# Kernel tuning notes

Hardware: AMD Instinct MI355X
Metric: run time of the kernel (lower is better)

## Reference

```python
import jax, jax.numpy as jnp
import numpy as np

N = 100000      # nodes
E = 3200000     # edges (before self-loops)
IN = 1          # input feature dim
H1, C = 4, 8    # layer1: 4 heads x 8 channels; layer2: 1 head x 8 channels
NEG_SLOPE = 0.2


def setup_inputs() -> dict:
    key = jax.random.key(0)
    ks = jax.random.split(key, 10)
    x = jax.random.normal(ks[0], (N, IN), jnp.float32)
    edge_index = jax.random.randint(ks[1], (2, E), 0, N, dtype=jnp.int32)
    # layer 1 params (GATConv(1, 8, heads=4))
    W1 = jax.random.normal(ks[2], (IN, H1 * C), jnp.float32) * 0.5
    a_src1 = jax.random.normal(ks[3], (H1, C), jnp.float32) * 0.5
    a_dst1 = jax.random.normal(ks[4], (H1, C), jnp.float32) * 0.5
    b1 = jnp.zeros((H1 * C,), jnp.float32)
    # layer 2 params (GATConv(32, 8, heads=1))
    W2 = jax.random.normal(ks[5], (H1 * C, C), jnp.float32) * 0.2
    a_src2 = jax.random.normal(ks[6], (1, C), jnp.float32) * 0.5
    a_dst2 = jax.random.normal(ks[7], (1, C), jnp.float32) * 0.5
    b2 = jnp.zeros((C,), jnp.float32)
    return {"x": x, "edge_index": edge_index, "W1": W1, "a_src1": a_src1,
            "a_dst1": a_dst1, "b1": b1, "W2": W2, "a_src2": a_src2,
            "a_dst2": a_dst2, "b2": b2}


def _gat_layer(x, src, dst, W, a_s, a_d, b, heads, ch):
    # Linear transform per head: [N, heads, ch]
    h = (x @ W).reshape(-1, heads, ch)
    # per-node attention logits
    al_s = jnp.einsum('nhc,hc->nh', h, a_s)  # [N, H]
    al_d = jnp.einsum('nhc,hc->nh', h, a_d)  # [N, H]
    # per-edge logits (message src -> dst)
    e = jax.nn.leaky_relu(al_s[src] + al_d[dst], NEG_SLOPE)  # [E', H]
    # segment softmax over incoming edges of each dst node
    m = jax.ops.segment_max(e, dst, num_segments=N)          # [N, H]
    e = jnp.exp(e - m[dst])
    s = jax.ops.segment_sum(e, dst, num_segments=N)          # [N, H]
    alpha = e / s[dst]                                       # [E', H]
    # weighted scatter-add aggregation
    out = jax.ops.segment_sum(h[src] * alpha[:, :, None], dst, num_segments=N)
    return out.reshape(N, heads * ch) + b


def reference(x, edge_index, W1, a_src1, a_dst1, b1, W2, a_src2, a_dst2, b2):
    loops = jnp.arange(N, dtype=edge_index.dtype)
    src = jnp.concatenate([edge_index[0], loops])  # add self-loops (PyG default)
    dst = jnp.concatenate([edge_index[1], loops])
    h = _gat_layer(x, src, dst, W1, a_src1, a_dst1, b1, H1, C)
    h = jax.nn.relu(h)
    out = _gat_layer(h, src, dst, W2, a_src2, a_dst2, b2, 1, C)
    return out
```

## Files before the change

### kernel.cpp

```cpp
#include <hip/hip_runtime.h>
#include <hip/hip_bf16.h>

#define NEG_SLOPE 0.2f
#define CAP   6144
#define CAPG  8192
#define CAPA  81920


__global__ void init_cc(int* __restrict__ curA, int* __restrict__ curB,
                        const float* __restrict__ W1,
                        const float* __restrict__ as1,
                        const float* __restrict__ ad1,
                        float* __restrict__ consts) {
    int t = threadIdx.x;
    if (t < 8) {
        int h = t & 3;
        const float* a = (t < 4) ? as1 : ad1;
        float s = 0.f;
        #pragma unroll
        for (int c = 0; c < 8; ++c)
            s += W1[h * 8 + c] * a[h * 8 + c];
        consts[t] = s;
    }
    if (t < 64) curA[t] = t * CAPA;
    curB[t] = t << 13;
}

__global__ void scatterA(const int* __restrict__ ei, int* __restrict__ curA,
                         unsigned int* __restrict__ bufA, int E) {
    __shared__ int cnt[64];
    __shared__ int basel[64];
    int t = threadIdx.x;
    int chunk = (E + gridDim.x - 1) / gridDim.x;
    int lo = blockIdx.x * chunk;
    int hi = min(E, lo + chunk);
    const int* dei = ei + E;
    if (t < 64) cnt[t] = 0;
    __syncthreads();
    bool vec = ((E & 3) == 0);
    int lo4 = (lo + 3) & ~3;
    int end4 = hi & ~3;
    if (vec && end4 > lo4) {
        for (int e = lo + t; e < lo4; e += 1024)
            atomicAdd(&cnt[dei[e] >> 11], 1);
        const int4* dei4 = (const int4*)dei;
        for (int v = (lo4 >> 2) + t; v < (end4 >> 2); v += 1024) {
            int4 d = dei4[v];
            atomicAdd(&cnt[d.x >> 11], 1);
            atomicAdd(&cnt[d.y >> 11], 1);
            atomicAdd(&cnt[d.z >> 11], 1);
            atomicAdd(&cnt[d.w >> 11], 1);
        }
        for (int e = end4 + t; e < hi; e += 1024)
            atomicAdd(&cnt[dei[e] >> 11], 1);
    } else {
        for (int e = lo + t; e < hi; e += 1024)
            atomicAdd(&cnt[dei[e] >> 11], 1);
    }
    __syncthreads();
    if (t < 64) {
        int c = cnt[t];
        basel[t] = c ? (atomicAdd(&curA[t], c) - t * CAPA) : 0;
        cnt[t] = 0;
    }
    __syncthreads();
    if (vec && end4 > lo4) {
        for (int e = lo + t; e < lo4; e += 1024) {
            int s = ei[e], d = dei[e];
            int sp = d >> 11;
            int off = basel[sp] + atomicAdd(&cnt[sp], 1);
            if (off < CAPA) bufA[sp * CAPA + off] = (unsigned)s | ((unsigned)(d & 2047) << 17);
        }
        const int4* sei4 = (const int4*)ei;
        const int4* dei4 = (const int4*)dei;
        for (int v = (lo4 >> 2) + t; v < (end4 >> 2); v += 1024) {
            int4 sv = sei4[v];
            int4 dv = dei4[v];
            int s0 = dv.x >> 11, s1 = dv.y >> 11, s2 = dv.z >> 11, s3 = dv.w >> 11;
            int o0 = basel[s0] + atomicAdd(&cnt[s0], 1);
            if (o0 < CAPA) bufA[s0 * CAPA + o0] = (unsigned)sv.x | ((unsigned)(dv.x & 2047) << 17);
            int o1 = basel[s1] + atomicAdd(&cnt[s1], 1);
            if (o1 < CAPA) bufA[s1 * CAPA + o1] = (unsigned)sv.y | ((unsigned)(dv.y & 2047) << 17);
            int o2 = basel[s2] + atomicAdd(&cnt[s2], 1);
            if (o2 < CAPA) bufA[s2 * CAPA + o2] = (unsigned)sv.z | ((unsigned)(dv.z & 2047) << 17);
            int o3 = basel[s3] + atomicAdd(&cnt[s3], 1);
            if (o3 < CAPA) bufA[s3 * CAPA + o3] = (unsigned)sv.w | ((unsigned)(dv.w & 2047) << 17);
        }
        for (int e = end4 + t; e < hi; e += 1024) {
            int s = ei[e], d = dei[e];
            int sp = d >> 11;
            int off = basel[sp] + atomicAdd(&cnt[sp], 1);
            if (off < CAPA) bufA[sp * CAPA + off] = (unsigned)s | ((unsigned)(d & 2047) << 17);
        }
    } else {
        for (int e = lo + t; e < hi; e += 1024) {
            int s = ei[e], d = dei[e];
            int sp = d >> 11;
            int off = basel[sp] + atomicAdd(&cnt[sp], 1);
            if (off < CAPA) bufA[sp * CAPA + off] = (unsigned)s | ((unsigned)(d & 2047) << 17);
        }
    }
}

__global__ void scatterB(const int* __restrict__ curA, int* __restrict__ curB,
                         const unsigned int* __restrict__ bufA,
                         unsigned int* __restrict__ pairs) {
    __shared__ int cnt[16];
    __shared__ int basel[16];
    int t = threadIdx.x;
    int sp = blockIdx.x >> 3;
    int part = blockIdx.x & 7;
    int base = sp * CAPA;
    int fill = min(curA[sp] - base, CAPA);
    if (fill <= 0) return;
    int lo = (fill * part) >> 3;
    int hi = (fill * (part + 1)) >> 3;
    for (int c0 = lo; c0 < hi; c0 += 8192) {
        int cend = min(hi, c0 + 8192);
        if (t < 16) cnt[t] = 0;
        __syncthreads();
        for (int i = c0 + t; i < cend; i += 1024)
            atomicAdd(&cnt[(bufA[base + i] >> 24) & 15], 1);
        __syncthreads();
        if (t < 16) {
            int c = cnt[t];
            int bkg = (sp << 4) + t;
            basel[t] = c ? (atomicAdd(&curB[bkg], c) - (bkg << 13)) : 0;
            cnt[t] = 0;
        }
        __syncthreads();
        for (int i = c0 + t; i < cend; i += 1024) {
            unsigned p = bufA[base + i];
            int b16 = (p >> 24) & 15;
            int off = basel[b16] + atomicAdd(&cnt[b16], 1);
            if (off < CAPG) {
                int bkg = (sp << 4) + b16;
                pairs[(bkg << 13) + off] = p & 0x00FFFFFFu;
            }
        }
        __syncthreads();
    }
}

__global__ __launch_bounds__(1024, 8)
void l1_comb(const float* __restrict__ x,
             const int* __restrict__ curB,
             const unsigned int* __restrict__ pairs,
             const float* __restrict__ consts,
             const float* __restrict__ W1, const float* __restrict__ b1,
             const float* __restrict__ W2,
             const float* __restrict__ as2, const float* __restrict__ ad2,
             float* __restrict__ h2, float* __restrict__ als2,
             float* __restrict__ ald2, int N) {
    __shared__ unsigned sbuf[CAP];
    __shared__ int hcnt[128], offs[128], hcur[128];
    __shared__ float xl[128];
    int t = threadIdx.x;
    int bk = blockIdx.x;
    int node0 = bk << 7;
    int nw = min(128, N - node0);
    if (t < 128) xl[t] = (t < nw) ? x[node0 + t] : 0.f;
    float S[4], D[4];
    #pragma unroll
    for (int h = 0; h < 4; ++h) { S[h] = consts[h]; D[h] = consts[4 + h]; }
    int base = bk << 13;
    int cnt_total = min(curB[bk] - base, CAPG);
    int g = t >> 3, j = t & 7;
    float sacc[4] = {0.f, 0.f, 0.f, 0.f};
    float tacc[4] = {0.f, 0.f, 0.f, 0.f};
    __syncthreads();
    float xd = xl[g];
    for (int c0 = 0; c0 < cnt_total; c0 += CAP) {
        int clen = min(CAP, cnt_total - c0);
        unsigned pr[6];
        #pragma unroll
        for (int k = 0; k < 6; ++k) {
            int idx = t + (k << 10);
            pr[k] = (idx < clen) ? pairs[base + c0 + idx] : 0xFFFFFFFFu;
        }
        if (t < 128) hcnt[t] = 0;
        __syncthreads();
        #pragma unroll
        for (int k = 0; k < 6; ++k)
            if (pr[k] != 0xFFFFFFFFu) atomicAdd(&hcnt[pr[k] >> 17], 1);
        __syncthreads();
        if (t < 64) {
            int h0 = hcnt[2 * t], h1 = hcnt[2 * t + 1];
            int s = h0 + h1, sc_ = s;
            #pragma unroll
            for (int o = 1; o < 64; o <<= 1) {
                int u = __shfl_up(sc_, o);
                if (t >= o) sc_ += u;
            }
            int excl = sc_ - s;
            offs[2 * t] = excl;          hcur[2 * t] = excl;
            offs[2 * t + 1] = excl + h0; hcur[2 * t + 1] = excl + h0;
        }
        __syncthreads();
        #pragma unroll
        for (int k = 0; k < 6; ++k)
            if (pr[k] != 0xFFFFFFFFu) {
                int loc = atomicAdd(&hcur[pr[k] >> 17], 1);
                sbuf[loc] = pr[k];
            }
        __syncthreads();
        int st = offs[g], en = st + hcnt[g];
        int i = st + j;
        float xs0 = 0.f, xs1 = 0.f;
        if (i < en) xs0 = x[sbuf[i] & 131071u];
        if (i + 8 < en) xs1 = x[sbuf[i + 8] & 131071u];
        for (; i < en; i += 8) {
            float xs = xs0;
            xs0 = xs1;
            int i2 = i + 16;
            xs1 = (i2 < en) ? x[sbuf[i2] & 131071u] : 0.f;
            #pragma unroll
            for (int h = 0; h < 4; ++h) {
                float v = xs * S[h] + xd * D[h];
                v = (v > 0.f) ? v : NEG_SLOPE * v;
                float w = __expf(v);
                sacc[h] += w;
                tacc[h] = fmaf(w, xs, tacc[h]);
            }
        }
        __syncthreads();
    }
    #pragma unroll
    for (int h = 0; h < 4; ++h) {
        sacc[h] += __shfl_xor(sacc[h], 1); sacc[h] += __shfl_xor(sacc[h], 2);
        sacc[h] += __shfl_xor(sacc[h], 4);
        tacc[h] += __shfl_xor(tacc[h], 1); tacc[h] += __shfl_xor(tacc[h], 2);
        tacc[h] += __shfl_xor(tacc[h], 4);
    }
    if (j == 0 && g < nw) {
        int n = node0 + g;
        float xn = xd;
        float o[8];
        #pragma unroll
        for (int c = 0; c < 8; ++c) o[c] = 0.f;
        #pragma unroll
        for (int h = 0; h < 4; ++h) {
            float v = xn * (S[h] + D[h]);
            v = (v > 0.f) ? v : NEG_SLOPE * v;
            float ww = __expf(v);
            float s1 = ww + sacc[h];
            float t1 = ww * xn + tacc[h];
            float tt = t1 / s1;
            #pragma unroll
            for (int c = 0; c < 8; ++c) {
                float rr = fmaxf(tt * W1[h * 8 + c] + b1[h * 8 + c], 0.f);
                #pragma unroll
                for (int c2 = 0; c2 < 8; ++c2) o[c2] += rr * W2[(h * 8 + c) * 8 + c2];
            }
        }
        float as = 0.f, ad = 0.f;
        #pragma unroll
        for (int c = 0; c < 8; ++c) { as += o[c] * as2[c]; ad += o[c] * ad2[c]; }
        float4* hv = (float4*)&h2[(size_t)n * 8];
        hv[0] = make_float4(o[0], o[1], o[2], o[3]);
        hv[1] = make_float4(o[4], o[5], o[6], o[7]);
        als2[n] = as;
        ald2[n] = ad;
    }
}

__global__ __launch_bounds__(1024, 8)
void l2_comb(const int* __restrict__ curB,
             const unsigned int* __restrict__ pairs,
             const float* __restrict__ als2, const float* __restrict__ ald2,
             const float* __restrict__ h2, const float* __restrict__ b2,
             float* __restrict__ out, int N) {
    __shared__ unsigned sbuf[CAP];
    __shared__ int hcnt[128], offs[128], hcur[128];
    __shared__ float adl[128];
    int t = threadIdx.x;
    int bk = blockIdx.x;
    int node0 = bk << 7;
    int nw = min(128, N - node0);
    if (t < 128) adl[t] = (t < nw) ? ald2[node0 + t] : 0.f;
    int base = bk << 13;
    int cnt_total = min(curB[bk] - base, CAPG);
    int g = t >> 3, j = t & 7;
    float acc[9];
    #pragma unroll
    for (int c = 0; c < 9; ++c) acc[c] = 0.f;
    __syncthreads();
    float adv = adl[g];
    for (int c0 = 0; c0 < cnt_total; c0 += CAP) {
        int clen = min(CAP, cnt_total - c0);
        unsigned pr[6];
        #pragma unroll
        for (int k = 0; k < 6; ++k) {
            int idx = t + (k << 10);
            pr[k] = (idx < clen) ? pairs[base + c0 + idx] : 0xFFFFFFFFu;
        }
        if (t < 128) hcnt[t] = 0;
        __syncthreads();
        #pragma unroll
        for (int k = 0; k < 6; ++k)
            if (pr[k] != 0xFFFFFFFFu) atomicAdd(&hcnt[pr[k] >> 17], 1);
        __syncthreads();
        if (t < 64) {
            int h0 = hcnt[2 * t], h1 = hcnt[2 * t + 1];
            int s = h0 + h1, sc_ = s;
            #pragma unroll
            for (int o = 1; o < 64; o <<= 1) {
                int u = __shfl_up(sc_, o);
                if (t >= o) sc_ += u;
            }
            int excl = sc_ - s;
            offs[2 * t] = excl;          hcur[2 * t] = excl;
            offs[2 * t + 1] = excl + h0; hcur[2 * t + 1] = excl + h0;
        }
        __syncthreads();
        #pragma unroll
        for (int k = 0; k < 6; ++k)
            if (pr[k] != 0xFFFFFFFFu) {
                int loc = atomicAdd(&hcur[pr[k] >> 17], 1);
                sbuf[loc] = pr[k];
            }
        __syncthreads();
        int st = offs[g], en = st + hcnt[g];
        int i = st + j;
        float a0 = 0.f, a1 = 0.f;
        float4 hA0 = make_float4(0,0,0,0), hB0 = hA0, hA1 = hA0, hB1 = hA0;
        if (i < en) {
            int s0 = (int)(sbuf[i] & 131071u);
            a0 = als2[s0];
            const float4* q = (const float4*)&h2[(size_t)s0 * 8];
            hA0 = q[0]; hB0 = q[1];
        }
        if (i + 8 < en) {
            int s1 = (int)(sbuf[i + 8] & 131071u);
            a1 = als2[s1];
            const float4* q = (const float4*)&h2[(size_t)s1 * 8];
            hA1 = q[0]; hB1 = q[1];
        }
        for (; i < en; i += 8) {
            float a = a0; float4 hA = hA0, hB = hB0;
            a0 = a1; hA0 = hA1; hB0 = hB1;
            int i2 = i + 16;
            if (i2 < en) {
                int s2 = (int)(sbuf[i2] & 131071u);
                a1 = als2[s2];
                const float4* q = (const float4*)&h2[(size_t)s2 * 8];
                hA1 = q[0]; hB1 = q[1];
            } else {
                a1 = 0.f;
            }
            float v = a + adv;
            v = (v > 0.f) ? v : NEG_SLOPE * v;
            float w = __expf(v);
            acc[0] += w;
            acc[1] = fmaf(w, hA.x, acc[1]); acc[2] = fmaf(w, hA.y, acc[2]);
            acc[3] = fmaf(w, hA.z, acc[3]); acc[4] = fmaf(w, hA.w, acc[4]);
            acc[5] = fmaf(w, hB.x, acc[5]); acc[6] = fmaf(w, hB.y, acc[6]);
            acc[7] = fmaf(w, hB.z, acc[7]); acc[8] = fmaf(w, hB.w, acc[8]);
        }
        __syncthreads();
    }
    #pragma unroll
    for (int c = 0; c < 9; ++c) {
        acc[c] += __shfl_xor(acc[c], 1);
        acc[c] += __shfl_xor(acc[c], 2);
        acc[c] += __shfl_xor(acc[c], 4);
    }
    if (j == 0 && g < nw) {
        int n = node0 + g;
        float v = als2[n] + adv;
        v = (v > 0.f) ? v : NEG_SLOPE * v;
        float ww = __expf(v);
        const float4* hv = (const float4*)&h2[(size_t)n * 8];
        float4 ha0 = hv[0], hb0 = hv[1];
        float s2v = acc[0] + ww;
        float inv = 1.f / s2v;
        float4* ov = (float4*)&out[(size_t)n * 8];
        ov[0] = make_float4((acc[1] + ww * ha0.x) * inv + b2[0],
                            (acc[2] + ww * ha0.y) * inv + b2[1],
                            (acc[3] + ww * ha0.z) * inv + b2[2],
                            (acc[4] + ww * ha0.w) * inv + b2[3]);
        ov[1] = make_float4((acc[5] + ww * hb0.x) * inv + b2[4],
                            (acc[6] + ww * hb0.y) * inv + b2[5],
                            (acc[7] + ww * hb0.z) * inv + b2[6],
                            (acc[8] + ww * hb0.w) * inv + b2[7]);
    }
}


__global__ void prep_consts(const float* __restrict__ W1,
                            const float* __restrict__ as1,
                            const float* __restrict__ ad1,
                            float* __restrict__ consts) {
    int t = threadIdx.x;
    if (t >= 8) return;
    int h = t & 3;
    const float* a = (t < 4) ? as1 : ad1;
    float s = 0.f;
    #pragma unroll
    for (int c = 0; c < 8; ++c)
        s += W1[h * 8 + c] * a[h * 8 + c];
    consts[t] = s;
}

__global__ void edge_pass1(const int* __restrict__ ei, const float* __restrict__ x,
                           const float* __restrict__ consts,
                           float* __restrict__ s1, float* __restrict__ t1, int E, int N) {
    int e = blockIdx.x * blockDim.x + threadIdx.x;
    if (e >= E + N) return;
    int src, dst;
    if (e < E) { src = ei[e]; dst = ei[E + e]; }
    else       { src = dst = e - E; }
    float xs = x[src], xd = x[dst];
    #pragma unroll
    for (int h = 0; h < 4; ++h) {
        float v = xs * consts[h] + xd * consts[4 + h];
        v = (v > 0.f) ? v : NEG_SLOPE * v;
        float w = __expf(v);
        atomicAdd(&s1[dst * 4 + h], w);
        atomicAdd(&t1[dst * 4 + h], w * xs);
    }
}

__global__ void node_mid(const float* __restrict__ s1, const float* __restrict__ t1,
                         const float* __restrict__ W1, const float* __restrict__ b1,
                         const float* __restrict__ W2,
                         const float* __restrict__ as2, const float* __restrict__ ad2,
                         float* __restrict__ h2, float* __restrict__ als2,
                         float* __restrict__ ald2, int N) {
    int n = blockIdx.x * blockDim.x + threadIdx.x;
    if (n >= N) return;
    float o[8];
    #pragma unroll
    for (int c = 0; c < 8; ++c) o[c] = 0.f;
    #pragma unroll
    for (int h = 0; h < 4; ++h) {
        float t = t1[n * 4 + h] / s1[n * 4 + h];
        #pragma unroll
        for (int c = 0; c < 8; ++c) {
            float r = fmaxf(t * W1[h * 8 + c] + b1[h * 8 + c], 0.f);
            #pragma unroll
            for (int c2 = 0; c2 < 8; ++c2) o[c2] += r * W2[(h * 8 + c) * 8 + c2];
        }
    }
    float as = 0.f, ad = 0.f;
    #pragma unroll
    for (int c = 0; c < 8; ++c) { h2[n * 8 + c] = o[c]; as += o[c] * as2[c]; ad += o[c] * ad2[c]; }
    als2[n] = as; ald2[n] = ad;
}

__global__ void edge_pass2(const int* __restrict__ ei, const float* __restrict__ als2,
                           const float* __restrict__ ald2, const float* __restrict__ h2,
                           float* __restrict__ s2, float* __restrict__ acc2, int E, int N) {
    int e = blockIdx.x * blockDim.x + threadIdx.x;
    if (e >= E + N) return;
    int src, dst;
    if (e < E) { src = ei[e]; dst = ei[E + e]; }
    else       { src = dst = e - E; }
    float v = als2[src] + ald2[dst];
    v = (v > 0.f) ? v : NEG_SLOPE * v;
    float w = __expf(v);
    atomicAdd(&s2[dst], w);
    const float4* hs = (const float4*)&h2[src * 8];
    float4 a = hs[0], bq = hs[1];
    float* acc = &acc2[dst * 8];
    atomicAdd(&acc[0], w * a.x);  atomicAdd(&acc[1], w * a.y);
    atomicAdd(&acc[2], w * a.z);  atomicAdd(&acc[3], w * a.w);
    atomicAdd(&acc[4], w * bq.x); atomicAdd(&acc[5], w * bq.y);
    atomicAdd(&acc[6], w * bq.z); atomicAdd(&acc[7], w * bq.w);
}

__global__ void node_out(const float* __restrict__ s2, const float* __restrict__ acc2,
                         const float* __restrict__ b2, float* __restrict__ out, int N) {
    int i = blockIdx.x * blockDim.x + threadIdx.x;
    if (i >= N * 8) return;
    out[i] = acc2[i] / s2[i >> 3] + b2[i & 7];
}


extern "C" void kernel_launch(void* const* d_in, const int* in_sizes, int n_in,
                              void* d_out, int out_size, void* d_ws, size_t ws_size,
                              hipStream_t stream) {
    const float* x   = (const float*)d_in[0];
    const int*   ei  = (const int*)d_in[1];
    const float* W1  = (const float*)d_in[2];
    const float* as1 = (const float*)d_in[3];
    const float* ad1 = (const float*)d_in[4];
    const float* b1  = (const float*)d_in[5];
    const float* W2  = (const float*)d_in[6];
    const float* as2 = (const float*)d_in[7];
    const float* ad2 = (const float*)d_in[8];
    const float* b2  = (const float*)d_in[9];
    float* out = (float*)d_out;

    const int N = in_sizes[0];
    const int E = in_sizes[1] / 2;
    const int NBK = (N + 127) >> 7;

    float* ws = (float*)d_ws;
    size_t need = (size_t)(16 + 64 + 1024 + 10 * (size_t)N
                           + (size_t)1024 * CAPG + (size_t)64 * CAPA) * sizeof(float);

    if (N <= 131072 && ws_size >= need) {
        float*    consts = ws;
        int*      curA   = (int*)(ws + 16);
        int*      curB   = curA + 64;
        float*    als2   = ws + 16 + 64 + 1024;
        float*    ald2   = als2 + N;
        float*    h2     = ald2 + N;
        unsigned* pairs  = (unsigned*)(h2 + 8 * (size_t)N);
        unsigned* bufA   = pairs + (size_t)1024 * CAPG;

        init_cc<<<1, 1024, 0, stream>>>(curA, curB, W1, as1, ad1, consts);
        scatterA<<<256, 1024, 0, stream>>>(ei, curA, bufA, E);
        scatterB<<<512, 1024, 0, stream>>>(curA, curB, bufA, pairs);
        l1_comb<<<NBK, 1024, 0, stream>>>(x, curB, pairs, consts,
                                          W1, b1, W2, as2, ad2, h2, als2, ald2, N);
        l2_comb<<<NBK, 1024, 0, stream>>>(curB, pairs, als2, ald2, h2, b2, out, N);
    } else {
        float* consts = ws;
        float* s1   = ws + 16;
        float* t1   = s1 + 4 * (size_t)N;
        float* h2   = t1 + 4 * (size_t)N;
        float* als2 = h2 + 8 * (size_t)N;
        float* ald2 = als2 + (size_t)N;
        float* s2   = ald2 + (size_t)N;
        float* acc2 = s2 + (size_t)N;

        hipMemsetAsync(ws, 0, (16 + 8 * (size_t)N) * sizeof(float), stream);
        hipMemsetAsync(s2, 0, 9 * (size_t)N * sizeof(float), stream);
        prep_consts<<<1, 64, 0, stream>>>(W1, as1, ad1, consts);
        int total = E + N;
        edge_pass1<<<(total + 255) / 256, 256, 0, stream>>>(ei, x, consts, s1, t1, E, N);
        node_mid<<<(N + 255) / 256, 256, 0, stream>>>(s1, t1, W1, b1, W2, as2, ad2, h2, als2, ald2, N);
        edge_pass2<<<(total + 255) / 256, 256, 0, stream>>>(ei, als2, ald2, h2, s2, acc2, E, N);
        node_out<<<(N * 8 + 255) / 256, 256, 0, stream>>>(s2, acc2, b2, out, N);
    }
}
```

Baseline: 201.5 us.

## Fuse GAT pipeline into one cooperative kernel with grid syncs and reuse sorted edges

Merges the five separate launches (init, two scatter passes, layer-1 and layer-2 combines) into a single cooperative kernel separated by grid-wide syncs. Layer 1 now saves its per-block sorted edge lists and per-node offset/count metadata to global memory, so layer 2 reads them directly instead of re-histogramming and re-sorting in shared memory. The per-block chunk is enlarged to hold a full bucket in one pass. In exchange it adds grid-sync overhead, a persistent grid of 256 or 512 blocks looping over buckets, an occupancy query on the host, and a larger shared buffer that may reduce occupancy.

```diff
diff --git a/kernel.cpp b/kernel.cpp
--- a/kernel.cpp
+++ b/kernel.cpp
@@ -1,187 +1,177 @@
 #include <hip/hip_runtime.h>
+#include <hip/hip_cooperative_groups.h>
 #include <hip/hip_bf16.h>
 
+namespace cg = cooperative_groups;
+
 #define NEG_SLOPE 0.2f
-#define CAP   6144
-#define CAPG  8192
-#define CAPA  81920
-
-
-__global__ void init_cc(int* __restrict__ curA, int* __restrict__ curB,
-                        const float* __restrict__ W1,
-                        const float* __restrict__ as1,
-                        const float* __restrict__ ad1,
-                        float* __restrict__ consts) {
+#define CAPG 8192
+#define CAPA 81920
+
+
+__global__ __launch_bounds__(1024, 8)
+void fused_gat(const float* __restrict__ x, const int* __restrict__ ei,
+               const float* __restrict__ W1, const float* __restrict__ as1,
+               const float* __restrict__ ad1, const float* __restrict__ b1,
+               const float* __restrict__ W2, const float* __restrict__ as2,
+               const float* __restrict__ ad2, const float* __restrict__ b2,
+               float* __restrict__ out,
+               int* __restrict__ curA, int* __restrict__ curB,
+               unsigned* __restrict__ bufA, unsigned* __restrict__ pairs,
+               unsigned* __restrict__ gsorted, int* __restrict__ bmeta,
+               float* __restrict__ als2, float* __restrict__ ald2,
+               float* __restrict__ h2,
+               int E, int N, int nbk)
+{
+    cg::grid_group grid = cg::this_grid();
+    __shared__ unsigned sbuf[CAPG];
+    __shared__ int hcnt[128], offs[128], hcur[128];
+    __shared__ int cntA[64], baseA[64];
+    __shared__ int cntB[16], baseB[16];
+    __shared__ float xl[128];
+
     int t = threadIdx.x;
-    if (t < 8) {
-        int h = t & 3;
-        const float* a = (t < 4) ? as1 : ad1;
-        float s = 0.f;
-        #pragma unroll
-        for (int c = 0; c < 8; ++c)
-            s += W1[h * 8 + c] * a[h * 8 + c];
-        consts[t] = s;
-    }
-    if (t < 64) curA[t] = t * CAPA;
-    curB[t] = t << 13;
-}
-
-__global__ void scatterA(const int* __restrict__ ei, int* __restrict__ curA,
-                         unsigned int* __restrict__ bufA, int E) {
-    __shared__ int cnt[64];
-    __shared__ int basel[64];
-    int t = threadIdx.x;
-    int chunk = (E + gridDim.x - 1) / gridDim.x;
-    int lo = blockIdx.x * chunk;
-    int hi = min(E, lo + chunk);
-    const int* dei = ei + E;
-    if (t < 64) cnt[t] = 0;
-    __syncthreads();
-    bool vec = ((E & 3) == 0);
-    int lo4 = (lo + 3) & ~3;
-    int end4 = hi & ~3;
-    if (vec && end4 > lo4) {
-        for (int e = lo + t; e < lo4; e += 1024)
-            atomicAdd(&cnt[dei[e] >> 11], 1);
-        const int4* dei4 = (const int4*)dei;
-        for (int v = (lo4 >> 2) + t; v < (end4 >> 2); v += 1024) {
-            int4 d = dei4[v];
-            atomicAdd(&cnt[d.x >> 11], 1);
-            atomicAdd(&cnt[d.y >> 11], 1);
-            atomicAdd(&cnt[d.z >> 11], 1);
-            atomicAdd(&cnt[d.w >> 11], 1);
-        }
-        for (int e = end4 + t; e < hi; e += 1024)
-            atomicAdd(&cnt[dei[e] >> 11], 1);
-    } else {
-        for (int e = lo + t; e < hi; e += 1024)
-            atomicAdd(&cnt[dei[e] >> 11], 1);
-    }
-    __syncthreads();
-    if (t < 64) {
-        int c = cnt[t];
-        basel[t] = c ? (atomicAdd(&curA[t], c) - t * CAPA) : 0;
-        cnt[t] = 0;
-    }
-    __syncthreads();
-    if (vec && end4 > lo4) {
-        for (int e = lo + t; e < lo4; e += 1024) {
-            int s = ei[e], d = dei[e];
-            int sp = d >> 11;
-            int off = basel[sp] + atomicAdd(&cnt[sp], 1);
-            if (off < CAPA) bufA[sp * CAPA + off] = (unsigned)s | ((unsigned)(d & 2047) << 17);
-        }
-        const int4* sei4 = (const int4*)ei;
-        const int4* dei4 = (const int4*)dei;
-        for (int v = (lo4 >> 2) + t; v < (end4 >> 2); v += 1024) {
-            int4 sv = sei4[v];
-            int4 dv = dei4[v];
-            int s0 = dv.x >> 11, s1 = dv.y >> 11, s2 = dv.z >> 11, s3 = dv.w >> 11;
-            int o0 = basel[s0] + atomicAdd(&cnt[s0], 1);
-            if (o0 < CAPA) bufA[s0 * CAPA + o0] = (unsigned)sv.x | ((unsigned)(dv.x & 2047) << 17);
-            int o1 = basel[s1] + atomicAdd(&cnt[s1], 1);
-            if (o1 < CAPA) bufA[s1 * CAPA + o1] = (unsigned)sv.y | ((unsigned)(dv.y & 2047) << 17);
-            int o2 = basel[s2] + atomicAdd(&cnt[s2], 1);
-            if (o2 < CAPA) bufA[s2 * CAPA + o2] = (unsigned)sv.z | ((unsigned)(dv.z & 2047) << 17);
-            int o3 = basel[s3] + atomicAdd(&cnt[s3], 1);
-            if (o3 < CAPA) bufA[s3 * CAPA + o3] = (unsigned)sv.w | ((unsigned)(dv.w & 2047) << 17);
-        }
-        for (int e = end4 + t; e < hi; e += 1024) {
-            int s = ei[e], d = dei[e];
-            int sp = d >> 11;
-            int off = basel[sp] + atomicAdd(&cnt[sp], 1);
-            if (off < CAPA) bufA[sp * CAPA + off] = (unsigned)s | ((unsigned)(d & 2047) << 17);
-        }
-    } else {
-        for (int e = lo + t; e < hi; e += 1024) {
-            int s = ei[e], d = dei[e];
-            int sp = d >> 11;
-            int off = basel[sp] + atomicAdd(&cnt[sp], 1);
-            if (off < CAPA) bufA[sp * CAPA + off] = (unsigned)s | ((unsigned)(d & 2047) << 17);
-        }
-    }
-}
-
-__global__ void scatterB(const int* __restrict__ curA, int* __restrict__ curB,
-                         const unsigned int* __restrict__ bufA,
-                         unsigned int* __restrict__ pairs) {
-    __shared__ int cnt[16];
-    __shared__ int basel[16];
-    int t = threadIdx.x;
-    int sp = blockIdx.x >> 3;
-    int part = blockIdx.x & 7;
-    int base = sp * CAPA;
-    int fill = min(curA[sp] - base, CAPA);
-    if (fill <= 0) return;
-    int lo = (fill * part) >> 3;
-    int hi = (fill * (part + 1)) >> 3;
-    for (int c0 = lo; c0 < hi; c0 += 8192) {
-        int cend = min(hi, c0 + 8192);
-        if (t < 16) cnt[t] = 0;
-        __syncthreads();
-        for (int i = c0 + t; i < cend; i += 1024)
-            atomicAdd(&cnt[(bufA[base + i] >> 24) & 15], 1);
-        __syncthreads();
-        if (t < 16) {
-            int c = cnt[t];
-            int bkg = (sp << 4) + t;
-            basel[t] = c ? (atomicAdd(&curB[bkg], c) - (bkg << 13)) : 0;
-            cnt[t] = 0;
-        }
-        __syncthreads();
-        for (int i = c0 + t; i < cend; i += 1024) {
-            unsigned p = bufA[base + i];
-            int b16 = (p >> 24) & 15;
-            int off = basel[b16] + atomicAdd(&cnt[b16], 1);
-            if (off < CAPG) {
-                int bkg = (sp << 4) + b16;
-                pairs[(bkg << 13) + off] = p & 0x00FFFFFFu;
-            }
-        }
-        __syncthreads();
-    }
-}
-
-__global__ __launch_bounds__(1024, 8)
-void l1_comb(const float* __restrict__ x,
-             const int* __restrict__ curB,
-             const unsigned int* __restrict__ pairs,
-             const float* __restrict__ consts,
-             const float* __restrict__ W1, const float* __restrict__ b1,
-             const float* __restrict__ W2,
-             const float* __restrict__ as2, const float* __restrict__ ad2,
-             float* __restrict__ h2, float* __restrict__ als2,
-             float* __restrict__ ald2, int N) {
-    __shared__ unsigned sbuf[CAP];
-    __shared__ int hcnt[128], offs[128], hcur[128];
-    __shared__ float xl[128];
-    int t = threadIdx.x;
-    int bk = blockIdx.x;
-    int node0 = bk << 7;
-    int nw = min(128, N - node0);
-    if (t < 128) xl[t] = (t < nw) ? x[node0 + t] : 0.f;
+    int B = blockIdx.x;
+    int G = gridDim.x;
+
     float S[4], D[4];
     #pragma unroll
-    for (int h = 0; h < 4; ++h) { S[h] = consts[h]; D[h] = consts[4 + h]; }
-    int base = bk << 13;
-    int cnt_total = min(curB[bk] - base, CAPG);
-    int g = t >> 3, j = t & 7;
-    float sacc[4] = {0.f, 0.f, 0.f, 0.f};
-    float tacc[4] = {0.f, 0.f, 0.f, 0.f};
-    __syncthreads();
-    float xd = xl[g];
-    for (int c0 = 0; c0 < cnt_total; c0 += CAP) {
-        int clen = min(CAP, cnt_total - c0);
-        unsigned pr[6];
-        #pragma unroll
-        for (int k = 0; k < 6; ++k) {
+    for (int h = 0; h < 4; ++h) {
+        float s = 0.f, d = 0.f;
+        #pragma unroll
+        for (int c = 0; c < 8; ++c) {
+            float w = W1[h * 8 + c];
+            s += w * as1[h * 8 + c];
+            d += w * ad1[h * 8 + c];
+        }
+        S[h] = s; D[h] = d;
+    }
+
+    if (B == 0) {
+        if (t < 64) curA[t] = t * CAPA;
+        curB[t] = t << 13;
+    }
+    __threadfence();
+    grid.sync();
+
+    {
+        int chunk = (E + G - 1) / G;
+        int lo = B * chunk;
+        int hi = min(E, lo + chunk);
+        const int* dei = ei + E;
+        if (t < 64) cntA[t] = 0;
+        __syncthreads();
+        bool vec = ((E & 3) == 0);
+        int lo4 = (lo + 3) & ~3;
+        int end4 = hi & ~3;
+        if (vec && end4 > lo4) {
+            for (int e = lo + t; e < lo4; e += 1024) atomicAdd(&cntA[dei[e] >> 11], 1);
+            const int4* dei4 = (const int4*)dei;
+            for (int v = (lo4 >> 2) + t; v < (end4 >> 2); v += 1024) {
+                int4 d = dei4[v];
+                atomicAdd(&cntA[d.x >> 11], 1); atomicAdd(&cntA[d.y >> 11], 1);
+                atomicAdd(&cntA[d.z >> 11], 1); atomicAdd(&cntA[d.w >> 11], 1);
+            }
+            for (int e = end4 + t; e < hi; e += 1024) atomicAdd(&cntA[dei[e] >> 11], 1);
+        } else {
+            for (int e = lo + t; e < hi; e += 1024) atomicAdd(&cntA[dei[e] >> 11], 1);
+        }
+        __syncthreads();
+        if (t < 64) {
+            int c = cntA[t];
+            baseA[t] = c ? (atomicAdd(&curA[t], c) - t * CAPA) : 0;
+            cntA[t] = 0;
+        }
+        __syncthreads();
+        if (vec && end4 > lo4) {
+            for (int e = lo + t; e < lo4; e += 1024) {
+                int s = ei[e], d = dei[e]; int sp = d >> 11;
+                int off = baseA[sp] + atomicAdd(&cntA[sp], 1);
+                if (off < CAPA) bufA[sp * CAPA + off] = (unsigned)s | ((unsigned)(d & 2047) << 17);
+            }
+            const int4* sei4 = (const int4*)ei;
+            const int4* dei4 = (const int4*)dei;
+            for (int v = (lo4 >> 2) + t; v < (end4 >> 2); v += 1024) {
+                int4 sv = sei4[v]; int4 dv = dei4[v];
+                int s0 = dv.x >> 11, s1 = dv.y >> 11, s2 = dv.z >> 11, s3 = dv.w >> 11;
+                int o0 = baseA[s0] + atomicAdd(&cntA[s0], 1);
+                if (o0 < CAPA) bufA[s0 * CAPA + o0] = (unsigned)sv.x | ((unsigned)(dv.x & 2047) << 17);
+                int o1 = baseA[s1] + atomicAdd(&cntA[s1], 1);
+                if (o1 < CAPA) bufA[s1 * CAPA + o1] = (unsigned)sv.y | ((unsigned)(dv.y & 2047) << 17);
+                int o2 = baseA[s2] + atomicAdd(&cntA[s2], 1);
+                if (o2 < CAPA) bufA[s2 * CAPA + o2] = (unsigned)sv.z | ((unsigned)(dv.z & 2047) << 17);
+                int o3 = baseA[s3] + atomicAdd(&cntA[s3], 1);
+                if (o3 < CAPA) bufA[s3 * CAPA + o3] = (unsigned)sv.w | ((unsigned)(dv.w & 2047) << 17);
+            }
+            for (int e = end4 + t; e < hi; e += 1024) {
+                int s = ei[e], d = dei[e]; int sp = d >> 11;
+                int off = baseA[sp] + atomicAdd(&cntA[sp], 1);
+                if (off < CAPA) bufA[sp * CAPA + off] = (unsigned)s | ((unsigned)(d & 2047) << 17);
+            }
+        } else {
+            for (int e = lo + t; e < hi; e += 1024) {
+                int s = ei[e], d = dei[e]; int sp = d >> 11;
+                int off = baseA[sp] + atomicAdd(&cntA[sp], 1);
+                if (off < CAPA) bufA[sp * CAPA + off] = (unsigned)s | ((unsigned)(d & 2047) << 17);
+            }
+        }
+    }
+    __threadfence();
+    grid.sync();
+
+    {
+        int per = G >> 6;
+        int sp = B / per, part = B % per;
+        int base = sp * CAPA;
+        int fill = min(curA[sp] - base, CAPA);
+        if (fill > 0) {
+            int lo = (int)(((long long)fill * part) / per);
+            int hi = (int)(((long long)fill * (part + 1)) / per);
+            for (int c0 = lo; c0 < hi; c0 += 8192) {
+                int cend = min(hi, c0 + 8192);
+                if (t < 16) cntB[t] = 0;
+                __syncthreads();
+                for (int i = c0 + t; i < cend; i += 1024)
+                    atomicAdd(&cntB[(bufA[base + i] >> 24) & 15], 1);
+                __syncthreads();
+                if (t < 16) {
+                    int c = cntB[t];
+                    int bkg = (sp << 4) + t;
+                    baseB[t] = c ? (atomicAdd(&curB[bkg], c) - (bkg << 13)) : 0;
+                    cntB[t] = 0;
+                }
+                __syncthreads();
+                for (int i = c0 + t; i < cend; i += 1024) {
+                    unsigned p = bufA[base + i];
+                    int b16 = (p >> 24) & 15;
+                    int off = baseB[b16] + atomicAdd(&cntB[b16], 1);
+                    if (off < CAPG) pairs[(((sp << 4) + b16) << 13) + off] = p & 0x00FFFFFFu;
+                }
+                __syncthreads();
+            }
+        }
+    }
+    __threadfence();
+    grid.sync();
+
+    int g = t >> 3, jj = t & 7;
+    for (int bk = B; bk < nbk; bk += G) {
+        __syncthreads();
+        int node0 = bk << 7;
+        int nw = min(128, N - node0);
+        if (t < 128) xl[t] = (t < nw) ? x[node0 + t] : 0.f;
+        int base = bk << 13;
+        int clen = min(curB[bk] - base, CAPG);
+        unsigned pr[8];
+        #pragma unroll
+        for (int k = 0; k < 8; ++k) {
             int idx = t + (k << 10);
-            pr[k] = (idx < clen) ? pairs[base + c0 + idx] : 0xFFFFFFFFu;
+            pr[k] = (idx < clen) ? pairs[base + idx] : 0xFFFFFFFFu;
         }
         if (t < 128) hcnt[t] = 0;
         __syncthreads();
         #pragma unroll
-        for (int k = 0; k < 6; ++k)
+        for (int k = 0; k < 8; ++k)
             if (pr[k] != 0xFFFFFFFFu) atomicAdd(&hcnt[pr[k] >> 17], 1);
         __syncthreads();
         if (t < 64) {
@@ -198,14 +188,19 @@
         }
         __syncthreads();
         #pragma unroll
-        for (int k = 0; k < 6; ++k)
+        for (int k = 0; k < 8; ++k)
             if (pr[k] != 0xFFFFFFFFu) {
                 int loc = atomicAdd(&hcur[pr[k] >> 17], 1);
                 sbuf[loc] = pr[k];
             }
         __syncthreads();
+        for (int i = t; i < clen; i += 1024) gsorted[base + i] = sbuf[i];
+        if (t < 128) bmeta[(bk << 7) + t] = offs[t] | (hcnt[t] << 14);
+        float xd = xl[g];
+        float sacc[4] = {0.f, 0.f, 0.f, 0.f};
+        float tacc[4] = {0.f, 0.f, 0.f, 0.f};
         int st = offs[g], en = st + hcnt[g];
-        int i = st + j;
+        int i = st + jj;
         float xs0 = 0.f, xs1 = 0.f;
         if (i < en) xs0 = x[sbuf[i] & 131071u];
         if (i + 8 < en) xs1 = x[sbuf[i + 8] & 131071u];
@@ -223,125 +218,82 @@
                 tacc[h] = fmaf(w, xs, tacc[h]);
             }
         }
-        __syncthreads();
-    }
-    #pragma unroll
-    for (int h = 0; h < 4; ++h) {
-        sacc[h] += __shfl_xor(sacc[h], 1); sacc[h] += __shfl_xor(sacc[h], 2);
-        sacc[h] += __shfl_xor(sacc[h], 4);
-        tacc[h] += __shfl_xor(tacc[h], 1); tacc[h] += __shfl_xor(tacc[h], 2);
-        tacc[h] += __shfl_xor(tacc[h], 4);
-    }
-    if (j == 0 && g < nw) {
-        int n = node0 + g;
-        float xn = xd;
-        float o[8];
-        #pragma unroll
-        for (int c = 0; c < 8; ++c) o[c] = 0.f;
         #pragma unroll
         for (int h = 0; h < 4; ++h) {
-            float v = xn * (S[h] + D[h]);
-            v = (v > 0.f) ? v : NEG_SLOPE * v;
-            float ww = __expf(v);
-            float s1 = ww + sacc[h];
-            float t1 = ww * xn + tacc[h];
-            float tt = t1 / s1;
+            sacc[h] += __shfl_xor(sacc[h], 1); sacc[h] += __shfl_xor(sacc[h], 2);
+            sacc[h] += __shfl_xor(sacc[h], 4);
+            tacc[h] += __shfl_xor(tacc[h], 1); tacc[h] += __shfl_xor(tacc[h], 2);
+            tacc[h] += __shfl_xor(tacc[h], 4);
+        }
+        if (jj == 0 && g < nw) {
+            int n = node0 + g;
+            float xn = xd;
+            float o[8];
             #pragma unroll
-            for (int c = 0; c < 8; ++c) {
-                float rr = fmaxf(tt * W1[h * 8 + c] + b1[h * 8 + c], 0.f);
+            for (int c = 0; c < 8; ++c) o[c] = 0.f;
+            #pragma unroll
+            for (int h = 0; h < 4; ++h) {
+                float v = xn * (S[h] + D[h]);
+                v = (v > 0.f) ? v : NEG_SLOPE * v;
+                float ww = __expf(v);
+                float s1 = ww + sacc[h];
+                float t1 = ww * xn + tacc[h];
+                float tt = t1 / s1;
                 #pragma unroll
-                for (int c2 = 0; c2 < 8; ++c2) o[c2] += rr * W2[(h * 8 + c) * 8 + c2];
-            }
-        }
-        float as = 0.f, ad = 0.f;
-        #pragma unroll
-        for (int c = 0; c < 8; ++c) { as += o[c] * as2[c]; ad += o[c] * ad2[c]; }
-        float4* hv = (float4*)&h2[(size_t)n * 8];
-        hv[0] = make_float4(o[0], o[1], o[2], o[3]);
-        hv[1] = make_float4(o[4], o[5], o[6], o[7]);
-        als2[n] = as;
-        ald2[n] = ad;
-    }
-}
-
-__global__ __launch_bounds__(1024, 8)
-void l2_comb(const int* __restrict__ curB,
-             const unsigned int* __restrict__ pairs,
-             const float* __restrict__ als2, const float* __restrict__ ald2,
-             const float* __restrict__ h2, const float* __restrict__ b2,
-             float* __restrict__ out, int N) {
-    __shared__ unsigned sbuf[CAP];
-    __shared__ int hcnt[128], offs[128], hcur[128];
-    __shared__ float adl[128];
-    int t = threadIdx.x;
-    int bk = blockIdx.x;
-    int node0 = bk << 7;
-    int nw = min(128, N - node0);
-    if (t < 128) adl[t] = (t < nw) ? ald2[node0 + t] : 0.f;
-    int base = bk << 13;
-    int cnt_total = min(curB[bk] - base, CAPG);
-    int g = t >> 3, j = t & 7;
-    float acc[9];
-    #pragma unroll
-    for (int c = 0; c < 9; ++c) acc[c] = 0.f;
-    __syncthreads();
-    float adv = adl[g];
-    for (int c0 = 0; c0 < cnt_total; c0 += CAP) {
-        int clen = min(CAP, cnt_total - c0);
-        unsigned pr[6];
-        #pragma unroll
-        for (int k = 0; k < 6; ++k) {
-            int idx = t + (k << 10);
-            pr[k] = (idx < clen) ? pairs[base + c0 + idx] : 0xFFFFFFFFu;
-        }
-        if (t < 128) hcnt[t] = 0;
-        __syncthreads();
-        #pragma unroll
-        for (int k = 0; k < 6; ++k)
-            if (pr[k] != 0xFFFFFFFFu) atomicAdd(&hcnt[pr[k] >> 17], 1);
-        __syncthreads();
-        if (t < 64) {
-            int h0 = hcnt[2 * t], h1 = hcnt[2 * t + 1];
-            int s = h0 + h1, sc_ = s;
+                for (int c = 0; c < 8; ++c) {
+                    float rr = fmaxf(tt * W1[h * 8 + c] + b1[h * 8 + c], 0.f);
+                    #pragma unroll
+                    for (int c2 = 0; c2 < 8; ++c2) o[c2] += rr * W2[(h * 8 + c) * 8 + c2];
+                }
+            }
+            float as = 0.f, ad = 0.f;
             #pragma unroll
-            for (int o = 1; o < 64; o <<= 1) {
-                int u = __shfl_up(sc_, o);
-                if (t >= o) sc_ += u;
-            }
-            int excl = sc_ - s;
-            offs[2 * t] = excl;          hcur[2 * t] = excl;
-            offs[2 * t + 1] = excl + h0; hcur[2 * t + 1] = excl + h0;
-        }
-        __syncthreads();
-        #pragma unroll
-        for (int k = 0; k < 6; ++k)
-            if (pr[k] != 0xFFFFFFFFu) {
-                int loc = atomicAdd(&hcur[pr[k] >> 17], 1);
-                sbuf[loc] = pr[k];
-            }
-        __syncthreads();
-        int st = offs[g], en = st + hcnt[g];
-        int i = st + j;
+            for (int c = 0; c < 8; ++c) { as += o[c] * as2[c]; ad += o[c] * ad2[c]; }
+            float4* hv = (float4*)&h2[(size_t)n * 8];
+            hv[0] = make_float4(o[0], o[1], o[2], o[3]);
+            hv[1] = make_float4(o[4], o[5], o[6], o[7]);
+            als2[n] = as;
+            ald2[n] = ad;
+        }
+    }
+    __threadfence();
+    grid.sync();
+
+    for (int bk = B; bk < nbk; bk += G) {
+        __syncthreads();
+        int node0 = bk << 7;
+        int nw = min(128, N - node0);
+        if (t < 128) xl[t] = (t < nw) ? ald2[node0 + t] : 0.f;
+        __syncthreads();
+        int base = bk << 13;
+        float adv = xl[g];
+        int pk = bmeta[(bk << 7) + g];
+        int st = pk & 16383, cgn = pk >> 14;
+        const unsigned* run = gsorted + base + st;
+        float acc[9];
+        #pragma unroll
+        for (int c = 0; c < 9; ++c) acc[c] = 0.f;
+        int i = jj;
         float a0 = 0.f, a1 = 0.f;
         float4 hA0 = make_float4(0,0,0,0), hB0 = hA0, hA1 = hA0, hB1 = hA0;
-        if (i < en) {
-            int s0 = (int)(sbuf[i] & 131071u);
+        if (i < cgn) {
+            int s0 = (int)(run[i] & 131071u);
             a0 = als2[s0];
             const float4* q = (const float4*)&h2[(size_t)s0 * 8];
             hA0 = q[0]; hB0 = q[1];
         }
-        if (i + 8 < en) {
-            int s1 = (int)(sbuf[i + 8] & 131071u);
+        if (i + 8 < cgn) {
+            int s1 = (int)(run[i + 8] & 131071u);
             a1 = als2[s1];
             const float4* q = (const float4*)&h2[(size_t)s1 * 8];
             hA1 = q[0]; hB1 = q[1];
         }
-        for (; i < en; i += 8) {
+        for (; i < cgn; i += 8) {
             float a = a0; float4 hA = hA0, hB = hB0;
             a0 = a1; hA0 = hA1; hB0 = hB1;
             int i2 = i + 16;
-            if (i2 < en) {
-                int s2 = (int)(sbuf[i2] & 131071u);
+            if (i2 < cgn) {
+                int s2 = (int)(run[i2] & 131071u);
                 a1 = als2[s2];
                 const float4* q = (const float4*)&h2[(size_t)s2 * 8];
                 hA1 = q[0]; hB1 = q[1];
@@ -357,32 +309,31 @@
             acc[5] = fmaf(w, hB.x, acc[5]); acc[6] = fmaf(w, hB.y, acc[6]);
             acc[7] = fmaf(w, hB.z, acc[7]); acc[8] = fmaf(w, hB.w, acc[8]);
         }
-        __syncthreads();
-    }
-    #pragma unroll
-    for (int c = 0; c < 9; ++c) {
-        acc[c] += __shfl_xor(acc[c], 1);
-        acc[c] += __shfl_xor(acc[c], 2);
-        acc[c] += __shfl_xor(acc[c], 4);
-    }
-    if (j == 0 && g < nw) {
-        int n = node0 + g;
-        float v = als2[n] + adv;
-        v = (v > 0.f) ? v : NEG_SLOPE * v;
-        float ww = __expf(v);
-        const float4* hv = (const float4*)&h2[(size_t)n * 8];
-        float4 ha0 = hv[0], hb0 = hv[1];
-        float s2v = acc[0] + ww;
-        float inv = 1.f / s2v;
-        float4* ov = (float4*)&out[(size_t)n * 8];
-        ov[0] = make_float4((acc[1] + ww * ha0.x) * inv + b2[0],
-                            (acc[2] + ww * ha0.y) * inv + b2[1],
-                            (acc[3] + ww * ha0.z) * inv + b2[2],
-                            (acc[4] + ww * ha0.w) * inv + b2[3]);
-        ov[1] = make_float4((acc[5] + ww * hb0.x) * inv + b2[4],
-                            (acc[6] + ww * hb0.y) * inv + b2[5],
-                            (acc[7] + ww * hb0.z) * inv + b2[6],
-                            (acc[8] + ww * hb0.w) * inv + b2[7]);
+        #pragma unroll
+        for (int c = 0; c < 9; ++c) {
+            acc[c] += __shfl_xor(acc[c], 1);
+            acc[c] += __shfl_xor(acc[c], 2);
+            acc[c] += __shfl_xor(acc[c], 4);
+        }
+        if (jj == 0 && g < nw) {
+            int n = node0 + g;
+            float v = als2[n] + adv;
+            v = (v > 0.f) ? v : NEG_SLOPE * v;
+            float ww = __expf(v);
+            const float4* hv = (const float4*)&h2[(size_t)n * 8];
+            float4 ha0 = hv[0], hb0 = hv[1];
+            float s2v = acc[0] + ww;
+            float inv = 1.f / s2v;
+            float4* ov = (float4*)&out[(size_t)n * 8];
+            ov[0] = make_float4((acc[1] + ww * ha0.x) * inv + b2[0],
+                                (acc[2] + ww * ha0.y) * inv + b2[1],
+                                (acc[3] + ww * ha0.z) * inv + b2[2],
+                                (acc[4] + ww * ha0.w) * inv + b2[3]);
+            ov[1] = make_float4((acc[5] + ww * hb0.x) * inv + b2[4],
+                                (acc[6] + ww * hb0.y) * inv + b2[5],
+                                (acc[7] + ww * hb0.z) * inv + b2[6],
+                                (acc[8] + ww * hb0.w) * inv + b2[7]);
+        }
     }
 }
 
@@ -497,26 +448,40 @@
     const int NBK = (N + 127) >> 7;
 
     float* ws = (float*)d_ws;
-    size_t need = (size_t)(16 + 64 + 1024 + 10 * (size_t)N
-                           + (size_t)1024 * CAPG + (size_t)64 * CAPA) * sizeof(float);
-
+    size_t need = ((size_t)64 + 1024 + 131072 + 10 * (size_t)N
+                   + 2 * (size_t)1024 * CAPG + (size_t)64 * CAPA) * sizeof(float);
+
+    bool fused_ok = false;
     if (N <= 131072 && ws_size >= need) {
-        float*    consts = ws;
-        int*      curA   = (int*)(ws + 16);
-        int*      curB   = curA + 64;
-        float*    als2   = ws + 16 + 64 + 1024;
-        float*    ald2   = als2 + N;
-        float*    h2     = ald2 + N;
-        unsigned* pairs  = (unsigned*)(h2 + 8 * (size_t)N);
-        unsigned* bufA   = pairs + (size_t)1024 * CAPG;
-
-        init_cc<<<1, 1024, 0, stream>>>(curA, curB, W1, as1, ad1, consts);
-        scatterA<<<256, 1024, 0, stream>>>(ei, curA, bufA, E);
-        scatterB<<<512, 1024, 0, stream>>>(curA, curB, bufA, pairs);
-        l1_comb<<<NBK, 1024, 0, stream>>>(x, curB, pairs, consts,
-                                          W1, b1, W2, as2, ad2, h2, als2, ald2, N);
-        l2_comb<<<NBK, 1024, 0, stream>>>(curB, pairs, als2, ald2, h2, b2, out, N);
-    } else {
+        int*      curA    = (int*)ws;
+        int*      curB    = curA + 64;
+        int*      bmeta   = curB + 1024;
+        float*    als2    = (float*)(bmeta + 131072);
+        float*    ald2    = als2 + N;
+        float*    h2      = ald2 + N;
+        unsigned* pairs   = (unsigned*)(h2 + 8 * (size_t)N);
+        unsigned* gsorted = pairs + (size_t)1024 * CAPG;
+        unsigned* bufA    = gsorted + (size_t)1024 * CAPG;
+
+        int maxb = 0;
+        hipError_t qerr = hipOccupancyMaxActiveBlocksPerMultiprocessor(
+            &maxb, (const void*)fused_gat, 1024, 0);
+        int gridsz = (qerr == hipSuccess && maxb >= 2) ? 512 : 256;
+
+        int e_ = E, n_ = N, nbk_ = NBK;
+        void* args[] = { (void*)&x, (void*)&ei, (void*)&W1, (void*)&as1,
+                         (void*)&ad1, (void*)&b1, (void*)&W2, (void*)&as2,
+                         (void*)&ad2, (void*)&b2, (void*)&out,
+                         (void*)&curA, (void*)&curB, (void*)&bufA,
+                         (void*)&pairs, (void*)&gsorted, (void*)&bmeta,
+                         (void*)&als2, (void*)&ald2, (void*)&h2,
+                         (void*)&e_, (void*)&n_, (void*)&nbk_ };
+        hipError_t lerr = hipLaunchCooperativeKernel(
+            (const void*)fused_gat, dim3(gridsz), dim3(1024), args, 0, stream);
+        fused_ok = (lerr == hipSuccess);
+    }
+
+    if (!fused_ok) {
         float* consts = ws;
         float* s1   = ws + 16;
         float* t1   = s1 + 4 * (size_t)N;
```

New measurement: 705.1 us. 250% more time.
